# Kernel tuning notes

Measured on AMD Instinct MI355X. Metric: run time of the kernel, lower is better.

Reference implementation:

```python
import jax, jax.numpy as jnp
import numpy as np

N, C, H, W = 4, 256, 64, 64
C_EMBED = C // 2  # 128

def setup_inputs() -> dict:
    key = jax.random.key(0)
    k1, k2, k3, k4 = jax.random.split(key, 4)
    x = jax.random.normal(k1, (N, C, H, W), dtype=jnp.float32)
    # 1x1 conv weights stored as [out_ch, in_ch] (torch Conv2d weight squeezed)
    theta_w = jax.random.normal(k2, (C_EMBED, C), dtype=jnp.float32) * 0.01
    phi_w = jax.random.normal(k3, (C_EMBED, C), dtype=jnp.float32) * 0.01
    proj_w = jax.random.normal(k4, (C, C), dtype=jnp.float32) * 0.01
    return {"x": x, "theta_w": theta_w, "phi_w": phi_w, "proj_w": proj_w}

def reference(x, theta_w, phi_w, proj_w):
    n, c, h, w = x.shape
    s = h * w
    xf = x.reshape(n, c, s)  # [n, c, s]
    theta = jnp.einsum('ec,ncs->nse', theta_w, xf)  # [n, s, e]
    phi = jnp.einsum('ec,ncs->nes', phi_w, xf)      # [n, e, s]
    scale = jnp.sqrt(jnp.float32(theta_w.shape[0]))
    f = jnp.einsum('nse,net->nst', theta, phi) / scale  # [n, s, s]
    f = jax.nn.softmax(f, axis=-1)
    y = jnp.einsum('nst,nct->ncs', f, xf)  # attend over g = x, -> [n, c, s]
    res = jnp.einsum('oc,ncs->nos', proj_w, y)  # 1x1 projection conv
    return x + res.reshape(n, c, h, w)
```

## Files before the change

### kernel.cpp

```cpp
#include <hip/hip_runtime.h>
#include <cstdint>
#include <cstddef>

#define NB 4
#define CH 256
#define SS 4096
#define EE 128
#define QSCALE 0.08838834764831845f

typedef __attribute__((ext_vector_type(8))) short bfrag;
typedef __attribute__((ext_vector_type(8))) unsigned short u16x8;
typedef __attribute__((ext_vector_type(4))) float f32x4;

__device__ __forceinline__ unsigned short f2bf(float f) {
  union { float f; unsigned int u; } v; v.f = f;
  unsigned int u = v.u;
  unsigned int r = u + 0x7FFFu + ((u >> 16) & 1u);
  return (unsigned short)(r >> 16);
}

__global__ __launch_bounds__(256) void cvt_w(
    const float* __restrict__ thw, const float* __restrict__ phw,
    const float* __restrict__ pw,
    unsigned short* __restrict__ thwb, unsigned short* __restrict__ phwb,
    unsigned short* __restrict__ pwb)
{
  const int nw4 = EE * CH / 4;
  const int np4 = CH * CH / 4;
  int i = blockIdx.x * 256 + threadIdx.x;
  const float* src; unsigned short* dst; int off;
  if      (i < nw4)           { src = thw; dst = thwb; off = i; }
  else if (i < 2 * nw4)       { src = phw; dst = phwb; off = i - nw4; }
  else if (i < 2 * nw4 + np4) { src = pw;  dst = pwb;  off = i - 2 * nw4; }
  else return;
  float4 v = reinterpret_cast<const float4*>(src)[off];
  ushort4 o;
  o.x = f2bf(v.x); o.y = f2bf(v.y); o.z = f2bf(v.z); o.w = f2bf(v.w);
  reinterpret_cast<ushort4*>(dst)[off] = o;
}

__global__ __launch_bounds__(512) void pass1_qk(
    const float* __restrict__ x,
    const unsigned short* __restrict__ thw,
    const unsigned short* __restrict__ phw,
    unsigned short* __restrict__ xb,
    unsigned short* __restrict__ Qt,
    unsigned short* __restrict__ Kt)
{
  __shared__ unsigned short xT[64][CH + 8];
  const int t  = threadIdx.x;
  const int n  = blockIdx.y;
  const int s0 = blockIdx.x * 64;

  {
    const int soff = (t & 15) * 4;
    const int c0   = t >> 4;
    #pragma unroll
    for (int ci = 0; ci < 8; ++ci) {
      const int c = c0 + ci * 32;
      const size_t rowoff = ((size_t)n * CH + c) * SS + s0;
      float4 v = reinterpret_cast<const float4*>(x + rowoff)[soff >> 2];
      ushort4 o;
      o.x = f2bf(v.x); o.y = f2bf(v.y); o.z = f2bf(v.z); o.w = f2bf(v.w);
      reinterpret_cast<ushort4*>(xb + rowoff)[soff >> 2] = o;
      xT[soff + 0][c] = o.x;
      xT[soff + 1][c] = o.y;
      xT[soff + 2][c] = o.z;
      xT[soff + 3][c] = o.w;
    }
  }
  __syncthreads();

  const int w    = t >> 6;
  const int lane = t & 63;
  const int q    = lane >> 4;
  const int mr   = lane & 15;
  const int wrow = (w & 3) * 16;
  const int half = w >> 2;

  bfrag a[8];
  {
    const bfrag* rp = reinterpret_cast<const bfrag*>(&xT[wrow + mr][0]);
    #pragma unroll
    for (int k = 0; k < 8; ++k) a[k] = rp[k * 4 + q];
  }

  const unsigned short* wsel = half ? phw : thw;
  unsigned short*       osel = half ? Kt  : Qt;
  const float           sc   = half ? 1.0f : QSCALE;
  const bfrag* wp = reinterpret_cast<const bfrag*>(wsel);
  #pragma unroll
  for (int nt = 0; nt < 8; ++nt) {
    f32x4 acc = {0.f, 0.f, 0.f, 0.f};
    #pragma unroll
    for (int k = 0; k < 8; ++k) {
      bfrag b = wp[(nt * 16 + mr) * (CH / 8) + k * 4 + q];
      acc = __builtin_amdgcn_mfma_f32_16x16x32_bf16(a[k], b, acc, 0, 0, 0);
    }
    #pragma unroll
    for (int i = 0; i < 4; ++i) {
      const int srow = s0 + wrow + q * 4 + i;
      osel[((size_t)n * SS + srow) * EE + nt * 16 + mr] = f2bf(acc[i] * sc);
    }
  }
}

__global__ __launch_bounds__(512, 2) void pass2_attn(
    const unsigned short* __restrict__ Qt,
    const unsigned short* __restrict__ Kt,
    const unsigned short* __restrict__ xb,
    const unsigned short* __restrict__ pwb,
    const float* __restrict__ x,
    float* __restrict__ out)
{
  __shared__ __align__(16) unsigned char SMEM[51968];
  float          (*S_lds)[132] = reinterpret_cast<float(*)[132]>(SMEM);
  unsigned short (*P_lds)[136] = reinterpret_cast<unsigned short(*)[136]>(SMEM + 33792);
  float* row_m     = reinterpret_cast<float*>(SMEM + 51200);
  float* row_l     = reinterpret_cast<float*>(SMEM + 51456);
  float* row_alpha = reinterpret_cast<float*>(SMEM + 51712);

  const int t    = threadIdx.x;
  const int id   = blockIdx.x;
  const int xcd  = id & 7;
  const int n    = xcd >> 1;
  const int s0   = ((id >> 3) * 2 + (xcd & 1)) * 64;
  const int w    = t >> 6;
  const int lane = t & 63;
  const int q    = lane >> 4;
  const int mr   = lane & 15;

  if (t < 64) { row_m[t] = -INFINITY; row_l[t] = 0.f; }

  bfrag qa[4][4];
  #pragma unroll
  for (int ms = 0; ms < 4; ++ms) {
    const bfrag* rp = reinterpret_cast<const bfrag*>(
        Qt + ((size_t)n * SS + s0 + ms * 16 + mr) * EE);
    #pragma unroll
    for (int k = 0; k < 4; ++k) qa[ms][k] = rp[k * 4 + q];
  }

  f32x4 o_acc[4][2];
  #pragma unroll
  for (int ms = 0; ms < 4; ++ms)
    #pragma unroll
    for (int nt = 0; nt < 2; ++nt) o_acc[ms][nt] = (f32x4){0.f, 0.f, 0.f, 0.f};

  bfrag kb[4];
  {
    const bfrag* rp = reinterpret_cast<const bfrag*>(
        Kt + ((size_t)n * SS + w * 16 + mr) * EE);
    #pragma unroll
    for (int k = 0; k < 4; ++k) kb[k] = rp[k * 4 + q];
  }

  for (int t0 = 0; t0 < SS; t0 += 128) {
    bfrag vb[4][2];
    #pragma unroll
    for (int nt = 0; nt < 2; ++nt) {
      const int c = w * 32 + nt * 16 + mr;
      const bfrag* vp = reinterpret_cast<const bfrag*>(
          xb + ((size_t)n * CH + c) * SS + t0);
      #pragma unroll
      for (int kk = 0; kk < 4; ++kk) vb[kk][nt] = vp[kk * 4 + q];
    }

    #pragma unroll
    for (int ms = 0; ms < 4; ++ms) {
      f32x4 acc = {0.f, 0.f, 0.f, 0.f};
      #pragma unroll
      for (int k = 0; k < 4; ++k)
        acc = __builtin_amdgcn_mfma_f32_16x16x32_bf16(qa[ms][k], kb[k], acc, 0, 0, 0);
      #pragma unroll
      for (int i = 0; i < 4; ++i)
        S_lds[ms * 16 + q * 4 + i][w * 16 + mr] = acc[i];
    }
    __syncthreads();

    {
      const int t1 = t0 + 128;
      if (t1 < SS) {
        const bfrag* rp = reinterpret_cast<const bfrag*>(
            Kt + ((size_t)n * SS + t1 + w * 16 + mr) * EE);
        #pragma unroll
        for (int k = 0; k < 4; ++k) kb[k] = rp[k * 4 + q];
      }
    }

    {
      const int r  = t >> 3;
      const int cg = t & 7;
      const float4* srow = reinterpret_cast<const float4*>(&S_lds[r][cg * 16]);
      float4 v0 = srow[0], v1 = srow[1], v2 = srow[2], v3 = srow[3];
      float vmax = fmaxf(fmaxf(fmaxf(v0.x, v0.y), fmaxf(v0.z, v0.w)),
                         fmaxf(fmaxf(v1.x, v1.y), fmaxf(v1.z, v1.w)));
      vmax = fmaxf(vmax, fmaxf(fmaxf(fmaxf(v2.x, v2.y), fmaxf(v2.z, v2.w)),
                               fmaxf(fmaxf(v3.x, v3.y), fmaxf(v3.z, v3.w))));
      vmax = fmaxf(vmax, __shfl_xor(vmax, 1, 8));
      vmax = fmaxf(vmax, __shfl_xor(vmax, 2, 8));
      vmax = fmaxf(vmax, __shfl_xor(vmax, 4, 8));
      const float m_old = row_m[r];
      const float m_new = fmaxf(m_old, vmax);

      float p[16];
      p[0]=__expf(v0.x-m_new); p[1]=__expf(v0.y-m_new); p[2]=__expf(v0.z-m_new); p[3]=__expf(v0.w-m_new);
      p[4]=__expf(v1.x-m_new); p[5]=__expf(v1.y-m_new); p[6]=__expf(v1.z-m_new); p[7]=__expf(v1.w-m_new);
      p[8]=__expf(v2.x-m_new); p[9]=__expf(v2.y-m_new); p[10]=__expf(v2.z-m_new); p[11]=__expf(v2.w-m_new);
      p[12]=__expf(v3.x-m_new); p[13]=__expf(v3.y-m_new); p[14]=__expf(v3.z-m_new); p[15]=__expf(v3.w-m_new);
      float sum = 0.f;
      u16x8 pk0, pk1;
      #pragma unroll
      for (int j = 0; j < 8; ++j) { sum += p[j];     pk0[j] = f2bf(p[j]); }
      #pragma unroll
      for (int j = 0; j < 8; ++j) { sum += p[8 + j]; pk1[j] = f2bf(p[8 + j]); }
      *reinterpret_cast<u16x8*>(&P_lds[r][cg * 16])     = pk0;
      *reinterpret_cast<u16x8*>(&P_lds[r][cg * 16 + 8]) = pk1;
      sum += __shfl_xor(sum, 1, 8);
      sum += __shfl_xor(sum, 2, 8);
      sum += __shfl_xor(sum, 4, 8);
      if (cg == 0) {
        const float al = __expf(m_old - m_new);
        row_alpha[r] = al;
        row_m[r]     = m_new;
        row_l[r]     = row_l[r] * al + sum;
      }
    }
    __syncthreads();

    #pragma unroll
    for (int ms = 0; ms < 4; ++ms) {
      float al[4];
      #pragma unroll
      for (int i = 0; i < 4; ++i) al[i] = row_alpha[ms * 16 + q * 4 + i];
      #pragma unroll
      for (int nt = 0; nt < 2; ++nt)
        #pragma unroll
        for (int i = 0; i < 4; ++i) o_acc[ms][nt][i] *= al[i];
    }

    #pragma unroll
    for (int kk = 0; kk < 4; ++kk) {
      bfrag pa[4];
      #pragma unroll
      for (int ms = 0; ms < 4; ++ms)
        pa[ms] = reinterpret_cast<const bfrag*>(&P_lds[ms * 16 + mr][0])[kk * 4 + q];
      #pragma unroll
      for (int nt = 0; nt < 2; ++nt)
        #pragma unroll
        for (int ms = 0; ms < 4; ++ms)
          o_acc[ms][nt] = __builtin_amdgcn_mfma_f32_16x16x32_bf16(
              pa[ms], vb[kk][nt], o_acc[ms][nt], 0, 0, 0);
    }
  }

  __syncthreads();
  unsigned short (*Y_lds)[CH + 8] =
      reinterpret_cast<unsigned short(*)[CH + 8]>(SMEM);

  #pragma unroll
  for (int ms = 0; ms < 4; ++ms) {
    float inv[4];
    #pragma unroll
    for (int i = 0; i < 4; ++i) inv[i] = 1.0f / row_l[ms * 16 + q * 4 + i];
    #pragma unroll
    for (int nt = 0; nt < 2; ++nt) {
      const int c = w * 32 + nt * 16 + mr;
      #pragma unroll
      for (int i = 0; i < 4; ++i)
        Y_lds[ms * 16 + q * 4 + i][c] = f2bf(o_acc[ms][nt][i] * inv[i]);
    }
  }
  __syncthreads();

  #pragma unroll
  for (int ot = 0; ot < 2; ++ot) {
    const int o0 = w * 32 + ot * 16;
    bfrag a[8];
    {
      const bfrag* ap = reinterpret_cast<const bfrag*>(pwb + (o0 + mr) * CH);
      #pragma unroll
      for (int k = 0; k < 8; ++k) a[k] = ap[k * 4 + q];
    }
    #pragma unroll
    for (int st = 0; st < 4; ++st) {
      f32x4 acc = {0.f, 0.f, 0.f, 0.f};
      const bfrag* bp = reinterpret_cast<const bfrag*>(&Y_lds[st * 16 + mr][0]);
      #pragma unroll
      for (int k = 0; k < 8; ++k)
        acc = __builtin_amdgcn_mfma_f32_16x16x32_bf16(a[k], bp[k * 4 + q], acc, 0, 0, 0);
      #pragma unroll
      for (int i = 0; i < 4; ++i) {
        const int o = o0 + q * 4 + i;
        const int s = s0 + st * 16 + mr;
        const size_t idx = ((size_t)n * CH + o) * SS + s;
        out[idx] = x[idx] + acc[i];
      }
    }
  }
}

extern "C" void kernel_launch(void* const* d_in, const int* in_sizes, int n_in,
                              void* d_out, int out_size, void* d_ws, size_t ws_size,
                              hipStream_t stream) {
  const float* x   = (const float*)d_in[0];
  const float* thw = (const float*)d_in[1];
  const float* phw = (const float*)d_in[2];
  const float* pw  = (const float*)d_in[3];
  float* out = (float*)d_out;

  unsigned short* xb   = (unsigned short*)d_ws;
  unsigned short* Qt   = xb + (size_t)NB * CH * SS;
  unsigned short* Kt   = Qt + (size_t)NB * SS * EE;
  unsigned short* thwb = Kt + (size_t)NB * SS * EE;
  unsigned short* phwb = thwb + EE * CH;
  unsigned short* pwb  = phwb + EE * CH;

  const int nw4 = EE * CH / 4;
  const int np4 = CH * CH / 4;
  const int totw4 = 2 * nw4 + np4;
  cvt_w<<<(totw4 + 255) / 256, 256, 0, stream>>>(thw, phw, pw, thwb, phwb, pwb);

  pass1_qk  <<<dim3(SS / 64, NB), 512, 0, stream>>>(x, thwb, phwb, xb, Qt, Kt);
  pass2_attn<<<dim3(NB * SS / 64), 512, 0, stream>>>(Qt, Kt, xb, pwb, x, out);
}
```

Before: 196.4 us.

## Fuse weight conversion, QK projection and attention into one cooperative kernel

Replaces the three launches (weight conversion, Q/K projection, attention) with a single cooperative kernel that uses a grid-wide sync between the projection phase and the attention phase. Q is kept in LDS instead of being written to and re-read from global memory. The fp32 weights are converted to bf16 inline at each use. The aim is to remove launch gaps and the Q round trip. In exchange it adds a grid barrier, redundant per-block weight conversion, and a requirement that all 256 blocks be co-resident at 2 blocks per CU.

```diff
diff --git a/kernel.cpp b/kernel.cpp
--- a/kernel.cpp
+++ b/kernel.cpp
@@ -1,6 +1,9 @@
 #include <hip/hip_runtime.h>
+#include <hip/hip_cooperative_groups.h>
 #include <cstdint>
 #include <cstddef>
+
+namespace cg = cooperative_groups;
 
 #define NB 4
 #define CH 256
@@ -19,106 +22,16 @@
   return (unsigned short)(r >> 16);
 }
 
-__global__ __launch_bounds__(256) void cvt_w(
-    const float* __restrict__ thw, const float* __restrict__ phw,
+__global__ __launch_bounds__(512, 2) void fused_all(
+    const float* __restrict__ x,
+    const float* __restrict__ thw,
+    const float* __restrict__ phw,
     const float* __restrict__ pw,
-    unsigned short* __restrict__ thwb, unsigned short* __restrict__ phwb,
-    unsigned short* __restrict__ pwb)
-{
-  const int nw4 = EE * CH / 4;
-  const int np4 = CH * CH / 4;
-  int i = blockIdx.x * 256 + threadIdx.x;
-  const float* src; unsigned short* dst; int off;
-  if      (i < nw4)           { src = thw; dst = thwb; off = i; }
-  else if (i < 2 * nw4)       { src = phw; dst = phwb; off = i - nw4; }
-  else if (i < 2 * nw4 + np4) { src = pw;  dst = pwb;  off = i - 2 * nw4; }
-  else return;
-  float4 v = reinterpret_cast<const float4*>(src)[off];
-  ushort4 o;
-  o.x = f2bf(v.x); o.y = f2bf(v.y); o.z = f2bf(v.z); o.w = f2bf(v.w);
-  reinterpret_cast<ushort4*>(dst)[off] = o;
-}
-
-__global__ __launch_bounds__(512) void pass1_qk(
-    const float* __restrict__ x,
-    const unsigned short* __restrict__ thw,
-    const unsigned short* __restrict__ phw,
     unsigned short* __restrict__ xb,
-    unsigned short* __restrict__ Qt,
-    unsigned short* __restrict__ Kt)
-{
-  __shared__ unsigned short xT[64][CH + 8];
-  const int t  = threadIdx.x;
-  const int n  = blockIdx.y;
-  const int s0 = blockIdx.x * 64;
-
-  {
-    const int soff = (t & 15) * 4;
-    const int c0   = t >> 4;
-    #pragma unroll
-    for (int ci = 0; ci < 8; ++ci) {
-      const int c = c0 + ci * 32;
-      const size_t rowoff = ((size_t)n * CH + c) * SS + s0;
-      float4 v = reinterpret_cast<const float4*>(x + rowoff)[soff >> 2];
-      ushort4 o;
-      o.x = f2bf(v.x); o.y = f2bf(v.y); o.z = f2bf(v.z); o.w = f2bf(v.w);
-      reinterpret_cast<ushort4*>(xb + rowoff)[soff >> 2] = o;
-      xT[soff + 0][c] = o.x;
-      xT[soff + 1][c] = o.y;
-      xT[soff + 2][c] = o.z;
-      xT[soff + 3][c] = o.w;
-    }
-  }
-  __syncthreads();
-
-  const int w    = t >> 6;
-  const int lane = t & 63;
-  const int q    = lane >> 4;
-  const int mr   = lane & 15;
-  const int wrow = (w & 3) * 16;
-  const int half = w >> 2;
-
-  bfrag a[8];
-  {
-    const bfrag* rp = reinterpret_cast<const bfrag*>(&xT[wrow + mr][0]);
-    #pragma unroll
-    for (int k = 0; k < 8; ++k) a[k] = rp[k * 4 + q];
-  }
-
-  const unsigned short* wsel = half ? phw : thw;
-  unsigned short*       osel = half ? Kt  : Qt;
-  const float           sc   = half ? 1.0f : QSCALE;
-  const bfrag* wp = reinterpret_cast<const bfrag*>(wsel);
-  #pragma unroll
-  for (int nt = 0; nt < 8; ++nt) {
-    f32x4 acc = {0.f, 0.f, 0.f, 0.f};
-    #pragma unroll
-    for (int k = 0; k < 8; ++k) {
-      bfrag b = wp[(nt * 16 + mr) * (CH / 8) + k * 4 + q];
-      acc = __builtin_amdgcn_mfma_f32_16x16x32_bf16(a[k], b, acc, 0, 0, 0);
-    }
-    #pragma unroll
-    for (int i = 0; i < 4; ++i) {
-      const int srow = s0 + wrow + q * 4 + i;
-      osel[((size_t)n * SS + srow) * EE + nt * 16 + mr] = f2bf(acc[i] * sc);
-    }
-  }
-}
-
-__global__ __launch_bounds__(512, 2) void pass2_attn(
-    const unsigned short* __restrict__ Qt,
-    const unsigned short* __restrict__ Kt,
-    const unsigned short* __restrict__ xb,
-    const unsigned short* __restrict__ pwb,
-    const float* __restrict__ x,
+    unsigned short* __restrict__ Kt,
     float* __restrict__ out)
 {
   __shared__ __align__(16) unsigned char SMEM[51968];
-  float          (*S_lds)[132] = reinterpret_cast<float(*)[132]>(SMEM);
-  unsigned short (*P_lds)[136] = reinterpret_cast<unsigned short(*)[136]>(SMEM + 33792);
-  float* row_m     = reinterpret_cast<float*>(SMEM + 51200);
-  float* row_l     = reinterpret_cast<float*>(SMEM + 51456);
-  float* row_alpha = reinterpret_cast<float*>(SMEM + 51712);
 
   const int t    = threadIdx.x;
   const int id   = blockIdx.x;
@@ -130,16 +43,96 @@
   const int q    = lane >> 4;
   const int mr   = lane & 15;
 
+  {
+    unsigned short (*xT)[CH + 8] =
+        reinterpret_cast<unsigned short(*)[CH + 8]>(SMEM);
+    unsigned short (*Qlds)[136] =
+        reinterpret_cast<unsigned short(*)[136]>(SMEM + 33792);
+
+    {
+      const int soff = (t & 15) * 4;
+      const int c0   = t >> 4;
+      #pragma unroll
+      for (int ci = 0; ci < 8; ++ci) {
+        const int c = c0 + ci * 32;
+        const size_t rowoff = ((size_t)n * CH + c) * SS + s0;
+        float4 v = reinterpret_cast<const float4*>(x + rowoff)[soff >> 2];
+        ushort4 o;
+        o.x = f2bf(v.x); o.y = f2bf(v.y); o.z = f2bf(v.z); o.w = f2bf(v.w);
+        reinterpret_cast<ushort4*>(xb + rowoff)[soff >> 2] = o;
+        xT[soff + 0][c] = o.x;
+        xT[soff + 1][c] = o.y;
+        xT[soff + 2][c] = o.z;
+        xT[soff + 3][c] = o.w;
+      }
+    }
+    __syncthreads();
+
+    const int wrow = (w & 3) * 16;
+    const int half = w >> 2;
+
+    bfrag a[8];
+    {
+      const bfrag* rp = reinterpret_cast<const bfrag*>(&xT[wrow + mr][0]);
+      #pragma unroll
+      for (int k = 0; k < 8; ++k) a[k] = rp[k * 4 + q];
+    }
+
+    const float* wsel = half ? phw : thw;
+    #pragma unroll
+    for (int nt = 0; nt < 8; ++nt) {
+      f32x4 acc = {0.f, 0.f, 0.f, 0.f};
+      const float4* wr4 =
+          reinterpret_cast<const float4*>(wsel + (nt * 16 + mr) * CH);
+      #pragma unroll
+      for (int k = 0; k < 8; ++k) {
+        float4 w0 = wr4[(k * 4 + q) * 2];
+        float4 w1 = wr4[(k * 4 + q) * 2 + 1];
+        bfrag b;
+        b[0] = (short)f2bf(w0.x); b[1] = (short)f2bf(w0.y);
+        b[2] = (short)f2bf(w0.z); b[3] = (short)f2bf(w0.w);
+        b[4] = (short)f2bf(w1.x); b[5] = (short)f2bf(w1.y);
+        b[6] = (short)f2bf(w1.z); b[7] = (short)f2bf(w1.w);
+        acc = __builtin_amdgcn_mfma_f32_16x16x32_bf16(a[k], b, acc, 0, 0, 0);
+      }
+      if (half) {
+        #pragma unroll
+        for (int i = 0; i < 4; ++i) {
+          const int srow = s0 + wrow + q * 4 + i;
+          Kt[((size_t)n * SS + srow) * EE + nt * 16 + mr] = f2bf(acc[i]);
+        }
+      } else {
+        #pragma unroll
+        for (int i = 0; i < 4; ++i)
+          Qlds[wrow + q * 4 + i][nt * 16 + mr] = f2bf(acc[i] * QSCALE);
+      }
+    }
+    __syncthreads();
+  }
+
+  bfrag qa[4][4];
+  {
+    unsigned short (*Qlds)[136] =
+        reinterpret_cast<unsigned short(*)[136]>(SMEM + 33792);
+    #pragma unroll
+    for (int ms = 0; ms < 4; ++ms) {
+      const bfrag* rp = reinterpret_cast<const bfrag*>(&Qlds[ms * 16 + mr][0]);
+      #pragma unroll
+      for (int k = 0; k < 4; ++k) qa[ms][k] = rp[k * 4 + q];
+    }
+  }
+
+  float* row_m     = reinterpret_cast<float*>(SMEM + 51200);
+  float* row_l     = reinterpret_cast<float*>(SMEM + 51456);
+  float* row_alpha = reinterpret_cast<float*>(SMEM + 51712);
   if (t < 64) { row_m[t] = -INFINITY; row_l[t] = 0.f; }
 
-  bfrag qa[4][4];
-  #pragma unroll
-  for (int ms = 0; ms < 4; ++ms) {
-    const bfrag* rp = reinterpret_cast<const bfrag*>(
-        Qt + ((size_t)n * SS + s0 + ms * 16 + mr) * EE);
-    #pragma unroll
-    for (int k = 0; k < 4; ++k) qa[ms][k] = rp[k * 4 + q];
-  }
+  __threadfence();
+  cg::this_grid().sync();
+
+  float          (*S_lds)[132] = reinterpret_cast<float(*)[132]>(SMEM);
+  unsigned short (*P_lds)[136] =
+      reinterpret_cast<unsigned short(*)[136]>(SMEM + 33792);
 
   f32x4 o_acc[4][2];
   #pragma unroll
@@ -190,8 +183,8 @@
 
     {
       const int r  = t >> 3;
-      const int cg = t & 7;
-      const float4* srow = reinterpret_cast<const float4*>(&S_lds[r][cg * 16]);
+      const int cg_ = t & 7;
+      const float4* srow = reinterpret_cast<const float4*>(&S_lds[r][cg_ * 16]);
       float4 v0 = srow[0], v1 = srow[1], v2 = srow[2], v3 = srow[3];
       float vmax = fmaxf(fmaxf(fmaxf(v0.x, v0.y), fmaxf(v0.z, v0.w)),
                          fmaxf(fmaxf(v1.x, v1.y), fmaxf(v1.z, v1.w)));
@@ -214,12 +207,12 @@
       for (int j = 0; j < 8; ++j) { sum += p[j];     pk0[j] = f2bf(p[j]); }
       #pragma unroll
       for (int j = 0; j < 8; ++j) { sum += p[8 + j]; pk1[j] = f2bf(p[8 + j]); }
-      *reinterpret_cast<u16x8*>(&P_lds[r][cg * 16])     = pk0;
-      *reinterpret_cast<u16x8*>(&P_lds[r][cg * 16 + 8]) = pk1;
+      *reinterpret_cast<u16x8*>(&P_lds[r][cg_ * 16])     = pk0;
+      *reinterpret_cast<u16x8*>(&P_lds[r][cg_ * 16 + 8]) = pk1;
       sum += __shfl_xor(sum, 1, 8);
       sum += __shfl_xor(sum, 2, 8);
       sum += __shfl_xor(sum, 4, 8);
-      if (cg == 0) {
+      if (cg_ == 0) {
         const float al = __expf(m_old - m_new);
         row_alpha[r] = al;
         row_m[r]     = m_new;
@@ -278,9 +271,19 @@
     const int o0 = w * 32 + ot * 16;
     bfrag a[8];
     {
-      const bfrag* ap = reinterpret_cast<const bfrag*>(pwb + (o0 + mr) * CH);
-      #pragma unroll
-      for (int k = 0; k < 8; ++k) a[k] = ap[k * 4 + q];
+      const float4* ar4 =
+          reinterpret_cast<const float4*>(pw + (o0 + mr) * CH);
+      #pragma unroll
+      for (int k = 0; k < 8; ++k) {
+        float4 w0 = ar4[(k * 4 + q) * 2];
+        float4 w1 = ar4[(k * 4 + q) * 2 + 1];
+        bfrag b;
+        b[0] = (short)f2bf(w0.x); b[1] = (short)f2bf(w0.y);
+        b[2] = (short)f2bf(w0.z); b[3] = (short)f2bf(w0.w);
+        b[4] = (short)f2bf(w1.x); b[5] = (short)f2bf(w1.y);
+        b[6] = (short)f2bf(w1.z); b[7] = (short)f2bf(w1.w);
+        a[k] = b;
+      }
     }
     #pragma unroll
     for (int st = 0; st < 4; ++st) {
@@ -309,18 +312,11 @@
   const float* pw  = (const float*)d_in[3];
   float* out = (float*)d_out;
 
-  unsigned short* xb   = (unsigned short*)d_ws;
-  unsigned short* Qt   = xb + (size_t)NB * CH * SS;
-  unsigned short* Kt   = Qt + (size_t)NB * SS * EE;
-  unsigned short* thwb = Kt + (size_t)NB * SS * EE;
-  unsigned short* phwb = thwb + EE * CH;
-  unsigned short* pwb  = phwb + EE * CH;
-
-  const int nw4 = EE * CH / 4;
-  const int np4 = CH * CH / 4;
-  const int totw4 = 2 * nw4 + np4;
-  cvt_w<<<(totw4 + 255) / 256, 256, 0, stream>>>(thw, phw, pw, thwb, phwb, pwb);
-
-  pass1_qk  <<<dim3(SS / 64, NB), 512, 0, stream>>>(x, thwb, phwb, xb, Qt, Kt);
-  pass2_attn<<<dim3(NB * SS / 64), 512, 0, stream>>>(Qt, Kt, xb, pwb, x, out);
+  unsigned short* xb = (unsigned short*)d_ws;
+  unsigned short* Kt = xb + (size_t)NB * CH * SS;
+
+  void* args[] = {(void*)&x, (void*)&thw, (void*)&phw, (void*)&pw,
+                  (void*)&xb, (void*)&Kt, (void*)&out};
+  hipLaunchCooperativeKernel(reinterpret_cast<void*>(&fused_all),
+                             dim3(NB * SS / 64), dim3(512), args, 0, stream);
 }
```

After: 288.5 us. 1.47x slower.
